# Kernel optimization log

Hardware: AMD Instinct MI355X
Metric: run time of the kernel (lower is better)

## Reference

```python
import jax, jax.numpy as jnp
import numpy as np

B, NG, GS, D, L, NDL = 16, 50, 20, 256, 3, 2
N = NG * GS  # 1000


def setup_inputs() -> dict:
    key = jax.random.key(0)
    ks = jax.random.split(key, 8)
    amino_embd = jax.random.normal(ks[0], (B, NG, GS, D), dtype=jnp.float32)
    c = (jax.random.uniform(ks[1], (B, N, N)) < 0.02).astype(jnp.float32)
    prot_contacts = jnp.clip(c + jnp.transpose(c, (0, 2, 1)), 0.0, 1.0)
    # small init for bilinear W (original: random_uniform ~ +/-0.05) keeps exp() stable
    W_list = 0.01 * jax.random.normal(ks[2], (L, D, D), dtype=jnp.float32)
    dense_W = jax.random.normal(ks[3], (L, NDL, D, D), dtype=jnp.float32) / np.sqrt(D)
    dense_b = jnp.zeros((L, NDL, D), dtype=jnp.float32)
    final_W = jax.random.normal(ks[4], (D, D), dtype=jnp.float32) / np.sqrt(D)
    final_b = jnp.zeros((D,), dtype=jnp.float32)
    return {"amino_embd": amino_embd, "prot_contacts": prot_contacts,
            "W_list": W_list, "dense_W": dense_W, "dense_b": dense_b,
            "final_W": final_W, "final_b": final_b}


def reference(amino_embd, prot_contacts, W_list, dense_W, dense_b, final_W, final_b):
    dt = amino_embd.dtype
    eye = jnp.eye(N, dtype=dt)
    A = prot_contacts + eye  # contact map with self loops, [B,N,N]
    x = amino_embd.reshape(B, N, D)
    for l in range(L):
        x0 = x
        # bilinear non-local scores: [B,N,N]
        scores = jnp.einsum('bid,de,bje->bij', x0, W_list[l], x0)
        s = jnp.exp(scores) + jnp.asarray(1e-5, dt) * eye
        s = s * A                                   # mask by contacts + self loop
        s = s / jnp.sum(s, axis=-1, keepdims=True)  # row-normalize
        x = jnp.einsum('bij,bjd->bid', s, x0)       # aggregate
        for dl in range(NDL):
            x = jax.nn.relu(x @ dense_W[l, dl] + dense_b[l, dl])
        x = x + x0  # skip connection
    x = x @ final_W + final_b
    return x.reshape(B, NG, GS, D)
```

## Files before the change

kernel.cpp:

```cpp
#include <hip/hip_runtime.h>

#define BB 16
#define NN 1000
#define DD 256
#define LL 3
#define MAXNZ 256
#define MROWS (BB * NN)
#define SPLIT_SCALE 2048.0f
#define INV_SPLIT 4.8828125e-4f

typedef _Float16 f16x8 __attribute__((ext_vector_type(8)));
typedef _Float16 f16x2 __attribute__((ext_vector_type(2)));
typedef float f32x4 __attribute__((ext_vector_type(4)));

union H8 { f16x8 v; f16x2 p[4]; _Float16 h[8]; int4 i4; unsigned int w[4]; };

#if defined(__has_builtin)
#if __has_builtin(__builtin_amdgcn_fdot2)
#define HAS_FDOT2 1
#endif
#endif

__device__ __forceinline__ float dot2f(f16x2 a, f16x2 b, float c) {
#ifdef HAS_FDOT2
    return __builtin_amdgcn_fdot2(a, b, c, false);
#else
    return fmaf((float)a[0], (float)b[0], fmaf((float)a[1], (float)b[1], c));
#endif
}

__device__ __forceinline__ void fmix2(float& alo, float& ahi,
                                      unsigned int pk, float s) {
    asm("v_fma_mix_f32 %0, %1, %2, %0 op_sel:[0,0,0] op_sel_hi:[1,0,0]"
        : "+v"(alo) : "v"(pk), "v"(s));
    asm("v_fma_mix_f32 %0, %1, %2, %0 op_sel:[1,0,0] op_sel_hi:[1,0,0]"
        : "+v"(ahi) : "v"(pk), "v"(s));
}

__global__ __launch_bounds__(256) void setup_all(
    const float* __restrict__ W_list, const float* __restrict__ dense_W,
    const float* __restrict__ final_W,
    _Float16* __restrict__ wt_hi, _Float16* __restrict__ wt_lo,
    const float* __restrict__ x_in,
    _Float16* __restrict__ xh, _Float16* __restrict__ xl,
    const float* __restrict__ contacts,
    int* __restrict__ idx, int* __restrict__ cnt, float* __restrict__ adiag)
{
    __shared__ float T[64][68];
    int bid = blockIdx.x;
    int t = threadIdx.x;

    if (bid < 160) {
        int mat = bid >> 4;
        int tile = bid & 15;
        int tk = (tile >> 2) * 64, tn = (tile & 3) * 64;
        const float* src = (mat < 3) ? (W_list + (size_t)mat * 65536)
                         : (mat < 9) ? (dense_W + (size_t)(mat - 3) * 65536)
                                     : final_W;
        {
            int k = t >> 2, nc = (t & 3) * 16;
            const float* sp = src + (size_t)(tk + k) * 256 + tn + nc;
            *(float4*)&T[k][nc + 0]  = *(const float4*)(sp + 0);
            *(float4*)&T[k][nc + 4]  = *(const float4*)(sp + 4);
            *(float4*)&T[k][nc + 8]  = *(const float4*)(sp + 8);
            *(float4*)&T[k][nc + 12] = *(const float4*)(sp + 12);
        }
        __syncthreads();
        int n = t >> 2, kc = (t & 3) * 16;
        H8 hh0, hh1, ll0, ll1;
        #pragma unroll
        for (int i = 0; i < 16; ++i) {
            float x = T[kc + i][n];
            _Float16 hi = (_Float16)x;
            _Float16 lo = (_Float16)((x - (float)hi) * SPLIT_SCALE);
            if (i < 8) { hh0.h[i] = hi; ll0.h[i] = lo; }
            else       { hh1.h[i - 8] = hi; ll1.h[i - 8] = lo; }
        }
        size_t o = (size_t)mat * 65536 + (size_t)(tn + n) * 256 + tk + kc;
        *(int4*)(wt_hi + o)     = hh0.i4;
        *(int4*)(wt_hi + o + 8) = hh1.i4;
        *(int4*)(wt_lo + o)     = ll0.i4;
        *(int4*)(wt_lo + o + 8) = ll1.i4;
    } else if (bid < 2160) {
        size_t gid = (size_t)(bid - 160) * 256 + t;
        const float* p = x_in + gid * 8;
        float4 a = *(const float4*)p;
        float4 b = *(const float4*)(p + 4);
        float xs[8] = {a.x, a.y, a.z, a.w, b.x, b.y, b.z, b.w};
        H8 hh, ll;
        #pragma unroll
        for (int i = 0; i < 8; ++i) {
            _Float16 h = (_Float16)xs[i];
            hh.h[i] = h;
            ll.h[i] = (_Float16)((xs[i] - (float)h) * SPLIT_SCALE);
        }
        *(int4*)(xh + gid * 8) = hh.i4;
        *(int4*)(xl + gid * 8) = ll.i4;
    } else {
        int wave = (int)(((size_t)(bid - 2160) * 256 + t) >> 6);
        int lane = t & 63;
        int b = wave / NN;
        int i = wave - b * NN;
        const float* row = contacts + (size_t)b * NN * NN + (size_t)i * NN;
        int* out = idx + (size_t)wave * MAXNZ;
        int count = 0;
        for (int j0 = 0; j0 < NN; j0 += 64) {
            int j = j0 + lane;
            float v = (j < NN) ? row[j] : 0.0f;
            bool p = (v != 0.0f) && (j != i);
            unsigned long long bal = __ballot(p);
            if (p) {
                int pre = __popcll(bal & ((1ull << lane) - 1ull));
                out[count + pre] = j;
            }
            count += __popcll(bal);
        }
        if (lane == 0) {
            cnt[wave] = count;
            adiag[wave] = row[i] + 1.0f;
        }
    }
}

__global__ __launch_bounds__(256, 3) void sparse_agg(
    const _Float16* __restrict__ yhi,
    const _Float16* __restrict__ xhi, const _Float16* __restrict__ xlo,
    const int* __restrict__ idx, const int* __restrict__ cnt,
    const float* __restrict__ adiag,
    _Float16* __restrict__ ohi, _Float16* __restrict__ olo)
{
    int bid = blockIdx.x;
    int xcd = bid & 7;
    int chunk = bid >> 3;
    int row = xcd * 2000 + chunk * 4 + (int)(threadIdx.x >> 6);
    row = __builtin_amdgcn_readfirstlane(row);
    int lane = threadIdx.x & 63;
    int g = lane >> 4, s = lane & 15;
    int b = row / NN;

    const _Float16* yp = yhi + (size_t)row * DD + s * 8;
    H8 yh0, yh1;
    yh0.i4 = *(const int4*)yp;
    yh1.i4 = *(const int4*)(yp + 128);

    const _Float16* xph = xhi + (size_t)row * DD + s * 8;
    const _Float16* xpl = xlo + (size_t)row * DD + s * 8;
    H8 xih0, xih1, xil0, xil1;
    xih0.i4 = *(const int4*)xph;       xih1.i4 = *(const int4*)(xph + 128);
    xil0.i4 = *(const int4*)xpl;       xil1.i4 = *(const int4*)(xpl + 128);
    float xi[16];
    #pragma unroll
    for (int u = 0; u < 8; ++u) {
        xi[u]     = fmaf((float)xil0.h[u], INV_SPLIT, (float)xih0.h[u]);
        xi[8 + u] = fmaf((float)xil1.h[u], INV_SPLIT, (float)xih1.h[u]);
    }
    const _Float16* xb = xhi + (size_t)b * NN * DD;

    float p = 0.0f;
    #pragma unroll
    for (int u = 0; u < 8; ++u) {
        p = fmaf((float)yh0.h[u], xi[u], p);
        p = fmaf((float)yh1.h[u], xi[8 + u], p);
    }
    p += __shfl_xor(p, 1); p += __shfl_xor(p, 2);
    p += __shfl_xor(p, 4); p += __shfl_xor(p, 8);
    float wd = (g == 0) ? (__expf(p) + 1e-5f) * adiag[row] : 0.0f;
    float denom = wd;
    float acc[16];
    #pragma unroll
    for (int u = 0; u < 16; ++u) acc[u] = wd * xi[u];

    const int c = cnt[row];
    const int* ip = idx + (size_t)row * MAXNZ;
    const int iters = (c + 7) >> 3;

    int jA1, jB1;
    H8 vA0, vA1, vB0, vB1;
    {
        int ja = (g < c) ? ip[g] : 0;
        int jb = (4 + g < c) ? ip[4 + g] : 0;
        jA1 = (8 + g < c) ? ip[8 + g] : 0;
        jB1 = (12 + g < c) ? ip[12 + g] : 0;
        const _Float16* pa = xb + (size_t)ja * DD + s * 8;
        vA0.i4 = *(const int4*)pa;
        vA1.i4 = *(const int4*)(pa + 128);
        const _Float16* pb = xb + (size_t)jb * DD + s * 8;
        vB0.i4 = *(const int4*)pb;
        vB1.i4 = *(const int4*)(pb + 128);
    }

    for (int t = 0; t < iters; ++t) {
        int k2a = (t + 2) * 8 + g;
        int k2b = k2a + 4;
        int jA2 = (k2a < c) ? ip[k2a] : 0;
        int jB2 = (k2b < c) ? ip[k2b] : 0;
        H8 mA0, mA1, mB0, mB1;
        const _Float16* pa = xb + (size_t)jA1 * DD + s * 8;
        mA0.i4 = *(const int4*)pa;
        mA1.i4 = *(const int4*)(pa + 128);
        const _Float16* pb = xb + (size_t)jB1 * DD + s * 8;
        mB0.i4 = *(const int4*)pb;
        mB1.i4 = *(const int4*)(pb + 128);

        bool vokA = t * 8 + g < c;
        bool vokB = t * 8 + 4 + g < c;

        float qa0 = 0.0f, qa1 = 0.0f, qb0 = 0.0f, qb1 = 0.0f;
        #pragma unroll
        for (int i = 0; i < 4; ++i) {
            qa0 = dot2f(yh0.p[i], vA0.p[i], qa0);
            qa1 = dot2f(yh1.p[i], vA1.p[i], qa1);
            qb0 = dot2f(yh0.p[i], vB0.p[i], qb0);
            qb1 = dot2f(yh1.p[i], vB1.p[i], qb1);
        }
        float qa = qa0 + qa1, qb = qb0 + qb1;
        qa += __shfl_xor(qa, 1); qb += __shfl_xor(qb, 1);
        qa += __shfl_xor(qa, 2); qb += __shfl_xor(qb, 2);
        qa += __shfl_xor(qa, 4); qb += __shfl_xor(qb, 4);
        qa += __shfl_xor(qa, 8); qb += __shfl_xor(qb, 8);
        float wa = vokA ? __expf(qa) : 0.0f;
        float wb = vokB ? __expf(qb) : 0.0f;
        denom += wa + wb;
        #pragma unroll
        for (int i = 0; i < 4; ++i) {
            fmix2(acc[2 * i],     acc[2 * i + 1],     vA0.w[i], wa);
            fmix2(acc[8 + 2 * i], acc[8 + 2 * i + 1], vA1.w[i], wa);
        }
        #pragma unroll
        for (int i = 0; i < 4; ++i) {
            fmix2(acc[2 * i],     acc[2 * i + 1],     vB0.w[i], wb);
            fmix2(acc[8 + 2 * i], acc[8 + 2 * i + 1], vB1.w[i], wb);
        }

        vA0 = mA0; vA1 = mA1; vB0 = mB0; vB1 = mB1;
        jA1 = jA2; jB1 = jB2;
    }

#define XG(x) x += __shfl_xor(x, 16); x += __shfl_xor(x, 32);
    XG(denom);
    #pragma unroll
    for (int u = 0; u < 16; ++u) { XG(acc[u]) }
#undef XG

    float inv = 1.0f / denom;
    int half = (g & 1) * 8;
    H8 st;
    #pragma unroll
    for (int i = 0; i < 8; ++i) {
        float x = acc[half + i] * inv;
        _Float16 h = (_Float16)x;
        st.h[i] = (g & 2) ? (_Float16)((x - (float)h) * SPLIT_SCALE) : h;
    }
    _Float16* dst = ((g & 2) ? olo : ohi) + (size_t)row * DD + (g & 1) * 128 + s * 8;
    *(int4*)dst = st.i4;
}

__global__ __launch_bounds__(512, 4) void gemm16(
    const _Float16* __restrict__ Ahi, const _Float16* __restrict__ Alo,
    const _Float16* __restrict__ Bhi, const _Float16* __restrict__ Blo,
    const float* __restrict__ bias,
    const _Float16* __restrict__ Shi, const _Float16* __restrict__ Slo,
    _Float16* __restrict__ Chi, _Float16* __restrict__ Clo,
    float* __restrict__ Cf32, int relu, int lo_write)
{
    __shared__ __align__(16) char smem[49152];
    char* Ah = smem;
    char* Al = smem + 16384;
    char* Bh = smem + 32768;
    char* Bl = smem + 40960;

    int tid = threadIdx.x;
    int mBase = blockIdx.y * 128;
    int nBase = blockIdx.x * 64;

    int ra = tid >> 2, ka = (tid & 3) * 16;
    const _Float16* gAh = Ahi + (size_t)(mBase + ra) * 256 + ka;
    const _Float16* gAl = Alo + (size_t)(mBase + ra) * 256 + ka;
    int sbA = ra * 128 + ka * 2, swzA = (ra & 7) << 4;
    int rb = tid >> 3, kbb = (tid & 7) * 8;
    const _Float16* gBh = Bhi + (size_t)(nBase + rb) * 256 + kbb;
    const _Float16* gBl = Blo + (size_t)(nBase + rb) * 256 + kbb;
    int sbB = rb * 128 + kbb * 2, swzB = (rb & 7) << 4;

    int l = tid & 63, wv = tid >> 6;
    int wm = (wv & 3) * 32, wn = (wv >> 2) * 32;
    int lr = l & 15, lk = l >> 4;

    f32x4 acc0[2][2] = {};
    f32x4 acc1[2][2] = {};

    int4 rA0, rA1, rA2, rA3, rB0, rB1;
#define LOADG(kb) \
    rA0 = *(const int4*)(gAh + (kb));     rA1 = *(const int4*)(gAh + (kb) + 8); \
    rA2 = *(const int4*)(gAl + (kb));     rA3 = *(const int4*)(gAl + (kb) + 8); \
    rB0 = *(const int4*)(gBh + (kb));     rB1 = *(const int4*)(gBl + (kb));

    LOADG(0)

    #pragma unroll
    for (int kb = 0; kb < 256; kb += 64) {
        __syncthreads();
        *(int4*)(Ah + ((sbA +  0) ^ swzA)) = rA0;
        *(int4*)(Ah + ((sbA + 16) ^ swzA)) = rA1;
        *(int4*)(Al + ((sbA +  0) ^ swzA)) = rA2;
        *(int4*)(Al + ((sbA + 16) ^ swzA)) = rA3;
        *(int4*)(Bh + (sbB ^ swzB)) = rB0;
        *(int4*)(Bl + (sbB ^ swzB)) = rB1;
        __syncthreads();

        if (kb < 192) { LOADG(kb + 64) }

        #pragma unroll
        for (int kk = 0; kk < 2; ++kk) {
            int kby = kk * 64 + lk * 16;
            f16x8 fah[2], fal[2], fbh[2], fbl[2];
            #pragma unroll
            for (int mt = 0; mt < 2; ++mt) {
                int ml = wm + mt * 16 + lr;
                int off = (ml * 128 + kby) ^ ((ml & 7) << 4);
                fah[mt] = *(const f16x8*)(Ah + off);
                fal[mt] = *(const f16x8*)(Al + off);
            }
            #pragma unroll
            for (int nt = 0; nt < 2; ++nt) {
                int nl = wn + nt * 16 + lr;
                int off = (nl * 128 + kby) ^ ((nl & 7) << 4);
                fbh[nt] = *(const f16x8*)(Bh + off);
                fbl[nt] = *(const f16x8*)(Bl + off);
            }
            #pragma unroll
            for (int mt = 0; mt < 2; ++mt)
                #pragma unroll
                for (int nt = 0; nt < 2; ++nt) {
                    acc0[mt][nt] = __builtin_amdgcn_mfma_f32_16x16x32_f16(
                        fah[mt], fbh[nt], acc0[mt][nt], 0, 0, 0);
                    acc1[mt][nt] = __builtin_amdgcn_mfma_f32_16x16x32_f16(
                        fah[mt], fbl[nt], acc1[mt][nt], 0, 0, 0);
                    acc1[mt][nt] = __builtin_amdgcn_mfma_f32_16x16x32_f16(
                        fal[mt], fbh[nt], acc1[mt][nt], 0, 0, 0);
                }
        }
    }
#undef LOADG

    __syncthreads();
    float* T = (float*)smem;
    #pragma unroll
    for (int mt = 0; mt < 2; ++mt)
        #pragma unroll
        for (int nt = 0; nt < 2; ++nt)
            #pragma unroll
            for (int q = 0; q < 4; ++q) {
                int m = wm + mt * 16 + lk * 4 + q;
                int n = wn + nt * 16 + lr;
                T[m * 68 + n] = acc0[mt][nt][q] + acc1[mt][nt][q] * INV_SPLIT;
            }
    __syncthreads();

    {
        int rr = tid >> 2;
        int c0 = (tid & 3) * 16;
        int m = mBase + rr;
        size_t o = (size_t)m * 256 + nBase + c0;
        float v[16];
        #pragma unroll
        for (int i = 0; i < 4; ++i) {
            float4 f = *(const float4*)&T[rr * 68 + c0 + i * 4];
            v[i * 4 + 0] = f.x; v[i * 4 + 1] = f.y;
            v[i * 4 + 2] = f.z; v[i * 4 + 3] = f.w;
        }
        if (bias) {
            #pragma unroll
            for (int i = 0; i < 4; ++i) {
                float4 bv = *(const float4*)(bias + nBase + c0 + i * 4);
                v[i * 4 + 0] += bv.x; v[i * 4 + 1] += bv.y;
                v[i * 4 + 2] += bv.z; v[i * 4 + 3] += bv.w;
            }
        }
        if (relu) {
            #pragma unroll
            for (int i = 0; i < 16; ++i) v[i] = fmaxf(v[i], 0.0f);
        }
        if (Shi) {
            #pragma unroll
            for (int j = 0; j < 2; ++j) {
                H8 sh, sl;
                sh.i4 = *(const int4*)(Shi + o + j * 8);
                sl.i4 = *(const int4*)(Slo + o + j * 8);
                #pragma unroll
                for (int u = 0; u < 8; ++u)
                    v[j * 8 + u] += fmaf((float)sl.h[u], INV_SPLIT, (float)sh.h[u]);
            }
        }
        if (Cf32) {
            #pragma unroll
            for (int i = 0; i < 4; ++i) {
                *(float4*)(Cf32 + o + i * 4) =
                    make_float4(v[i * 4], v[i * 4 + 1], v[i * 4 + 2], v[i * 4 + 3]);
            }
        } else {
            #pragma unroll
            for (int j = 0; j < 2; ++j) {
                H8 hh;
                #pragma unroll
                for (int u = 0; u < 8; ++u) hh.h[u] = (_Float16)v[j * 8 + u];
                *(int4*)(Chi + o + j * 8) = hh.i4;
            }
            if (lo_write) {
                #pragma unroll
                for (int j = 0; j < 2; ++j) {
                    H8 ll;
                    #pragma unroll
                    for (int u = 0; u < 8; ++u) {
                        float x = v[j * 8 + u];
                        ll.h[u] = (_Float16)((x - (float)(_Float16)x) * SPLIT_SCALE);
                    }
                    *(int4*)(Clo + o + j * 8) = ll.i4;
                }
            }
        }
    }
}

extern "C" void kernel_launch(void* const* d_in, const int* in_sizes, int n_in,
                              void* d_out, int out_size, void* d_ws, size_t ws_size,
                              hipStream_t stream)
{
    const float* x_in     = (const float*)d_in[0];
    const float* contacts = (const float*)d_in[1];
    const float* W_list   = (const float*)d_in[2];
    const float* dense_W  = (const float*)d_in[3];
    const float* dense_b  = (const float*)d_in[4];
    const float* final_W  = (const float*)d_in[5];
    const float* final_b  = (const float*)d_in[6];
    float* out = (float*)d_out;

    char* ws = (char*)d_ws;
    const size_t PL = (size_t)MROWS * DD;
    _Float16* pl[8];
    for (int i = 0; i < 8; ++i) pl[i] = (_Float16*)ws + (size_t)i * PL;
    char* p8 = ws + 8 * PL * sizeof(_Float16);
    int*   idx   = (int*)p8;
    int*   cnt   = (int*)(p8 + (size_t)MROWS * MAXNZ * sizeof(int));
    float* adiag = (float*)((char*)cnt + (size_t)MROWS * sizeof(int));
    _Float16* wt_hi = (_Float16*)((char*)adiag + (size_t)MROWS * sizeof(float));
    _Float16* wt_lo = wt_hi + (size_t)10 * 65536;

    setup_all<<<6160, 256, 0, stream>>>(W_list, dense_W, final_W, wt_hi, wt_lo,
                                        x_in, pl[0], pl[1],
                                        contacts, idx, cnt, adiag);

    dim3 gg(4, MROWS / 128);
    int cur = 0;
    for (int l = 0; l < LL; ++l) {
        int oth = 1 - cur;
        _Float16 *x0h = pl[2 * cur], *x0l = pl[2 * cur + 1];
        _Float16 *yh  = pl[2 * oth], *yl  = pl[2 * oth + 1];
        _Float16 *xah = pl[4], *xal = pl[5];
        _Float16 *xbh = pl[6], *xbl = pl[7];
        gemm16<<<gg, 512, 0, stream>>>(x0h, x0l,
                                       wt_hi + (size_t)l * 65536,
                                       wt_lo + (size_t)l * 65536,
                                       nullptr, nullptr, nullptr,
                                       yh, yl, nullptr, 0, 0);
        sparse_agg<<<MROWS / 4, 256, 0, stream>>>(yh, x0h, x0l, idx, cnt, adiag,
                                                  xah, xal);
        gemm16<<<gg, 512, 0, stream>>>(xah, xal,
                                       wt_hi + (size_t)(3 + l * 2) * 65536,
                                       wt_lo + (size_t)(3 + l * 2) * 65536,
                                       dense_b + (size_t)(l * 2 + 0) * 256,
                                       nullptr, nullptr,
                                       xbh, xbl, nullptr, 1, 1);
        gemm16<<<gg, 512, 0, stream>>>(xbh, xbl,
                                       wt_hi + (size_t)(4 + l * 2) * 65536,
                                       wt_lo + (size_t)(4 + l * 2) * 65536,
                                       dense_b + (size_t)(l * 2 + 1) * 256,
                                       x0h, x0l,
                                       yh, yl, nullptr, 1, 1);
        cur = oth;
    }
    gemm16<<<gg, 512, 0, stream>>>(pl[2 * cur], pl[2 * cur + 1],
                                   wt_hi + (size_t)9 * 65536,
                                   wt_lo + (size_t)9 * 65536,
                                   final_b, nullptr, nullptr,
                                   nullptr, nullptr, out, 0, 0);
}
```

Before: 269.1 us.

## Fuse the two dense MLP GEMMs per layer into one kernel via LDS intermediate

Replaces the two back-to-back gemm16 launches for each layer's dense stack with a single mlp2 kernel. Each block computes a 64-row by 256-column tile of the first ReLU layer and keeps it in LDS as hi/lo fp16 splits, then runs the second GEMM with bias, ReLU and the residual add. This removes the global write and read of the intermediate activation and one launch per layer. In exchange it uses about 144KB of LDS per block, one block per CU, and a grid of only 250 blocks, which may lower occupancy and parallelism compared with the tiled gemm16 grid.

```diff
diff --git a/kernel.cpp b/kernel.cpp
--- a/kernel.cpp
+++ b/kernel.cpp
@@ -422,6 +422,162 @@
     }
 }
 
+__global__ __launch_bounds__(512, 1) void mlp2(
+    const _Float16* __restrict__ Ahi, const _Float16* __restrict__ Alo,
+    const _Float16* __restrict__ W1h, const _Float16* __restrict__ W1l,
+    const float* __restrict__ b1,
+    const _Float16* __restrict__ W2h, const _Float16* __restrict__ W2l,
+    const float* __restrict__ b2,
+    const _Float16* __restrict__ Shi, const _Float16* __restrict__ Slo,
+    _Float16* __restrict__ Chi, _Float16* __restrict__ Clo)
+{
+    __shared__ __align__(16) char smem[147456];
+    char* As  = smem;
+    char* Asl = smem + 8192;
+    char* Wp  = smem + 16384;
+    char* Wpl = smem + 49152;
+    char* H1h = smem + 81920;
+    char* H1l = smem + 114688;
+
+    int tid = threadIdx.x;
+    int mBase = blockIdx.x * 64;
+
+    int ra = tid >> 3, ka = (tid & 7) * 8;
+    const _Float16* gAh = Ahi + (size_t)(mBase + ra) * 256 + ka;
+    const _Float16* gAl = Alo + (size_t)(mBase + ra) * 256 + ka;
+    int sbA = ra * 128 + ka * 2, swA = (ra & 7) << 4;
+
+    int rw = tid >> 1, kw = (tid & 1) * 32;
+    int sbW = rw * 128 + kw * 2, swW = (rw & 7) << 4;
+
+    int l = tid & 63, wv = tid >> 6;
+    int wm = (wv & 1) * 32, wn = (wv >> 1) * 64;
+    int lr = l & 15, lk = l >> 4;
+
+    f32x4 acc0[2][4] = {};
+    f32x4 acc1[2][4] = {};
+
+    int4 pA0, pA1, pW[8];
+#define LA(kb) { pA0 = *(const int4*)(gAh + (kb)); pA1 = *(const int4*)(gAl + (kb)); }
+#define LW(Wh, Wl, kb) { \
+    const _Float16* _wh = (Wh) + (size_t)rw * 256 + kw + (kb); \
+    const _Float16* _wl = (Wl) + (size_t)rw * 256 + kw + (kb); \
+    pW[0] = *(const int4*)(_wh);      pW[1] = *(const int4*)(_wh + 8);  \
+    pW[2] = *(const int4*)(_wh + 16); pW[3] = *(const int4*)(_wh + 24); \
+    pW[4] = *(const int4*)(_wl);      pW[5] = *(const int4*)(_wl + 8);  \
+    pW[6] = *(const int4*)(_wl + 16); pW[7] = *(const int4*)(_wl + 24); }
+#define STW() \
+    *(int4*)(Wp  + ((sbW +  0) ^ swW)) = pW[0]; \
+    *(int4*)(Wp  + ((sbW + 16) ^ swW)) = pW[1]; \
+    *(int4*)(Wp  + ((sbW + 32) ^ swW)) = pW[2]; \
+    *(int4*)(Wp  + ((sbW + 48) ^ swW)) = pW[3]; \
+    *(int4*)(Wpl + ((sbW +  0) ^ swW)) = pW[4]; \
+    *(int4*)(Wpl + ((sbW + 16) ^ swW)) = pW[5]; \
+    *(int4*)(Wpl + ((sbW + 32) ^ swW)) = pW[6]; \
+    *(int4*)(Wpl + ((sbW + 48) ^ swW)) = pW[7];
+#define COMPUTE(ABASE_H, ABASE_L, RSTR, KOFF) \
+    _Pragma("unroll") \
+    for (int kk = 0; kk < 2; ++kk) { \
+        int kby = kk * 64 + lk * 16; \
+        f16x8 fah[2], fal[2], fbh[4], fbl[4]; \
+        _Pragma("unroll") \
+        for (int mt = 0; mt < 2; ++mt) { \
+            int ml = wm + mt * 16 + lr; \
+            int off = (ml * (RSTR) + (KOFF) + kby) ^ ((ml & 7) << 4); \
+            fah[mt] = *(const f16x8*)((ABASE_H) + off); \
+            fal[mt] = *(const f16x8*)((ABASE_L) + off); \
+        } \
+        _Pragma("unroll") \
+        for (int nt = 0; nt < 4; ++nt) { \
+            int nl = wn + nt * 16 + lr; \
+            int off = (nl * 128 + kby) ^ ((nl & 7) << 4); \
+            fbh[nt] = *(const f16x8*)(Wp + off); \
+            fbl[nt] = *(const f16x8*)(Wpl + off); \
+        } \
+        _Pragma("unroll") \
+        for (int mt = 0; mt < 2; ++mt) \
+            _Pragma("unroll") \
+            for (int nt = 0; nt < 4; ++nt) { \
+                acc0[mt][nt] = __builtin_amdgcn_mfma_f32_16x16x32_f16( \
+                    fah[mt], fbh[nt], acc0[mt][nt], 0, 0, 0); \
+                acc1[mt][nt] = __builtin_amdgcn_mfma_f32_16x16x32_f16( \
+                    fah[mt], fbl[nt], acc1[mt][nt], 0, 0, 0); \
+                acc1[mt][nt] = __builtin_amdgcn_mfma_f32_16x16x32_f16( \
+                    fal[mt], fbh[nt], acc1[mt][nt], 0, 0, 0); \
+            } \
+    }
+
+    LA(0) LW(W1h, W1l, 0)
+    #pragma unroll
+    for (int kb = 0; kb < 256; kb += 64) {
+        __syncthreads();
+        *(int4*)(As  + (sbA ^ swA)) = pA0;
+        *(int4*)(Asl + (sbA ^ swA)) = pA1;
+        STW()
+        __syncthreads();
+        if (kb < 192) { LA(kb + 64) LW(W1h, W1l, kb + 64) }
+        COMPUTE(As, Asl, 128, 0)
+    }
+
+    {
+        #pragma unroll
+        for (int mt = 0; mt < 2; ++mt)
+            #pragma unroll
+            for (int nt = 0; nt < 4; ++nt) {
+                int n = wn + nt * 16 + lr;
+                float bv = b1[n];
+                #pragma unroll
+                for (int q = 0; q < 4; ++q) {
+                    int m = wm + mt * 16 + lk * 4 + q;
+                    float v = acc0[mt][nt][q] + acc1[mt][nt][q] * INV_SPLIT + bv;
+                    v = fmaxf(v, 0.0f);
+                    _Float16 h = (_Float16)v;
+                    int off = (m * 512 + n * 2) ^ ((m & 7) << 4);
+                    *(_Float16*)(H1h + off) = h;
+                    *(_Float16*)(H1l + off) = (_Float16)((v - (float)h) * SPLIT_SCALE);
+                }
+                #pragma unroll
+                for (int q = 0; q < 4; ++q) {
+                    acc0[mt][nt][q] = 0.0f;
+                    acc1[mt][nt][q] = 0.0f;
+                }
+            }
+    }
+
+    LW(W2h, W2l, 0)
+    #pragma unroll
+    for (int kb = 0; kb < 256; kb += 64) {
+        __syncthreads();
+        STW()
+        __syncthreads();
+        if (kb < 192) { LW(W2h, W2l, kb + 64) }
+        COMPUTE(H1h, H1l, 512, kb * 2)
+    }
+
+    #pragma unroll
+    for (int mt = 0; mt < 2; ++mt)
+        #pragma unroll
+        for (int nt = 0; nt < 4; ++nt) {
+            int n = wn + nt * 16 + lr;
+            float bv = b2[n];
+            #pragma unroll
+            for (int q = 0; q < 4; ++q) {
+                int m = mBase + wm + mt * 16 + lk * 4 + q;
+                size_t o = (size_t)m * 256 + n;
+                float v = acc0[mt][nt][q] + acc1[mt][nt][q] * INV_SPLIT + bv;
+                v = fmaxf(v, 0.0f);
+                v += fmaf((float)Slo[o], INV_SPLIT, (float)Shi[o]);
+                _Float16 h = (_Float16)v;
+                Chi[o] = h;
+                Clo[o] = (_Float16)((v - (float)h) * SPLIT_SCALE);
+            }
+        }
+#undef LA
+#undef LW
+#undef STW
+#undef COMPUTE
+}
+
 extern "C" void kernel_launch(void* const* d_in, const int* in_sizes, int n_in,
                               void* d_out, int out_size, void* d_ws, size_t ws_size,
                               hipStream_t stream)
@@ -457,7 +613,6 @@
         _Float16 *x0h = pl[2 * cur], *x0l = pl[2 * cur + 1];
         _Float16 *yh  = pl[2 * oth], *yl  = pl[2 * oth + 1];
         _Float16 *xah = pl[4], *xal = pl[5];
-        _Float16 *xbh = pl[6], *xbl = pl[7];
         gemm16<<<gg, 512, 0, stream>>>(x0h, x0l,
                                        wt_hi + (size_t)l * 65536,
                                        wt_lo + (size_t)l * 65536,
@@ -465,18 +620,15 @@
                                        yh, yl, nullptr, 0, 0);
         sparse_agg<<<MROWS / 4, 256, 0, stream>>>(yh, x0h, x0l, idx, cnt, adiag,
                                                   xah, xal);
-        gemm16<<<gg, 512, 0, stream>>>(xah, xal,
-                                       wt_hi + (size_t)(3 + l * 2) * 65536,
-                                       wt_lo + (size_t)(3 + l * 2) * 65536,
-                                       dense_b + (size_t)(l * 2 + 0) * 256,
-                                       nullptr, nullptr,
-                                       xbh, xbl, nullptr, 1, 1);
-        gemm16<<<gg, 512, 0, stream>>>(xbh, xbl,
-                                       wt_hi + (size_t)(4 + l * 2) * 65536,
-                                       wt_lo + (size_t)(4 + l * 2) * 65536,
-                                       dense_b + (size_t)(l * 2 + 1) * 256,
-                                       x0h, x0l,
-                                       yh, yl, nullptr, 1, 1);
+        mlp2<<<MROWS / 64, 512, 0, stream>>>(xah, xal,
+                                             wt_hi + (size_t)(3 + l * 2) * 65536,
+                                             wt_lo + (size_t)(3 + l * 2) * 65536,
+                                             dense_b + (size_t)(l * 2 + 0) * 256,
+                                             wt_hi + (size_t)(4 + l * 2) * 65536,
+                                             wt_lo + (size_t)(4 + l * 2) * 65536,
+                                             dense_b + (size_t)(l * 2 + 1) * 256,
+                                             x0h, x0l,
+                                             yh, yl);
         cur = oth;
     }
     gemm16<<<gg, 512, 0, stream>>>(pl[2 * cur], pl[2 * cur + 1],
```

Result: slower. 321.7 us (+19.5%).
